# Kernel tuning notes

Hardware: AMD Instinct MI355X
Metric: run time of the kernel (lower is better)

Reference implementation:

```python
import jax, jax.numpy as jnp
import numpy as np

WIDTH = 1024
HEAD = 64


def setup_inputs() -> dict:
    key = jax.random.key(0)
    ks = jax.random.split(key, 8)
    B, S = 8, 2048
    x = jax.random.normal(ks[0], (B, S, WIDTH), dtype=jnp.float32)
    attn_mask = jnp.ones((B, S), dtype=jnp.int32)
    s = WIDTH ** -0.5
    Wq = jax.random.normal(ks[1], (WIDTH, HEAD), dtype=jnp.float32) * s
    bq = jnp.zeros((HEAD,), dtype=jnp.float32)
    Wk = jax.random.normal(ks[2], (WIDTH, HEAD), dtype=jnp.float32) * s
    bk = jnp.zeros((HEAD,), dtype=jnp.float32)
    Wv = jax.random.normal(ks[3], (WIDTH, HEAD), dtype=jnp.float32) * s
    bv = jnp.zeros((HEAD,), dtype=jnp.float32)
    return {"x": x, "attn_mask": attn_mask, "Wq": Wq, "bq": bq,
            "Wk": Wk, "bk": bk, "Wv": Wv, "bv": bv}


def reference(x, attn_mask, Wq, bq, Wk, bk, Wv, bv):
    # x: [B, S, width]; attn_mask: [B, S] (key padding mask)
    scale = HEAD ** -0.5
    Q = x @ Wq + bq  # [B, S, H]
    K = x @ Wk + bk
    V = x @ Wv + bv
    scores = jnp.einsum('bqh,bkh->bqk', Q, K) * scale  # [B, S, S]
    mask = (attn_mask[:, None, :] != 0)  # [B, 1, S] broadcast over queries
    scores = jnp.where(mask, scores, -jnp.inf)
    A = jax.nn.softmax(scores, axis=-1)
    return jnp.einsum('bqk,bkh->bqh', A, V)
```

## Files before the change

kernel.cpp:

```cpp
#include <hip/hip_runtime.h>
#include <hip/hip_bf16.h>

#define BATCH 8
#define SEQ   2048
#define DMODEL 1024
#define HD    64

typedef __attribute__((ext_vector_type(8))) short bf16x8;
typedef __attribute__((ext_vector_type(4))) float f32x4;
typedef __attribute__((ext_vector_type(4))) int int4v;
typedef __attribute__((ext_vector_type(2))) unsigned uint2v;
typedef unsigned int u32;

__device__ inline unsigned short f2bf(float f) {
    unsigned u = __builtin_bit_cast(unsigned, f);
    unsigned r = (u + 0x7FFFu + ((u >> 16) & 1u)) >> 16;
    return (unsigned short)r;
}

__device__ inline unsigned cvtpk(float lo, float hi) {
    unsigned r;
    asm("v_cvt_pk_bf16_f32 %0, %1, %2" : "=v"(r) : "v"(lo), "v"(hi));
    return r;
}

__device__ inline void gl_lds16(const void* g, void* l) {
    __builtin_amdgcn_global_load_lds(
        (const __attribute__((address_space(1))) u32*)g,
        (__attribute__((address_space(3))) u32*)l, 16, 0, 0);
}

__global__ void prep_w(const float* __restrict__ Wq, const float* __restrict__ Wk,
                       const float* __restrict__ Wv, unsigned short* __restrict__ WFrag) {
    __shared__ float tt[64][65];
    int p = blockIdx.x >> 4;
    int t = blockIdx.x & 15;
    int k0 = t * 64;
    const float* W = (p == 0) ? Wq : (p == 1) ? Wk : Wv;
    int tid = threadIdx.x;
#pragma unroll
    for (int j = 0; j < 16; j++) {
        int idx = tid + j * 256;
        int r = idx >> 6, c = idx & 63;
        tt[r][c] = W[(size_t)(k0 + r) * HD + c];
    }
    __syncthreads();
#pragma unroll
    for (int gi = 0; gi < 2; gi++) {
        int g = tid * 2 + gi;
        int ln = g & 15, lg = (g >> 4) & 3, s = (g >> 6) & 1, n = (g >> 7) & 3;
        union { bf16x8 v; unsigned short u[8]; } pk;
#pragma unroll
        for (int e = 0; e < 8; e++)
            pk.u[e] = f2bf(tt[s * 32 + lg * 8 + e][n * 16 + ln]);
        *(bf16x8*)(WFrag + (((size_t)(p * 4 + n) * 16 + t) * 1024 + s * 512 + lg * 128 + ln * 8)) = pk.v;
    }
}

__global__ __launch_bounds__(256, 2) void proj_kernel(
    const float* __restrict__ x,
    const float* __restrict__ bq, const float* __restrict__ bk, const float* __restrict__ bv,
    const unsigned short* __restrict__ WFrag,
    unsigned short* __restrict__ Q, unsigned short* __restrict__ K,
    unsigned short* __restrict__ VT) {

    __shared__ __align__(16) unsigned short Xls[32 * 1024];

    int tid = threadIdx.x;
    int w = tid >> 6, lane = tid & 63;
    int lg = lane >> 4, ln = lane & 15;
    int m0 = blockIdx.x * 32;

    const unsigned short* wbase[3];
#pragma unroll
    for (int j = 0; j < 3; j++)
        wbase[j] = WFrag + (size_t)(w * 3 + j) * 16384 + lane * 8;

#pragma unroll
    for (int j = 0; j < 16; j++) {
        int c = tid + j * 256;
        int row = c >> 7, slot = c & 127;
        const float* src = x + (size_t)(m0 + row) * DMODEL + slot * 8;
        f32x4 p0 = *(const f32x4*)(src);
        f32x4 p1 = *(const f32x4*)(src + 4);
        union { bf16x8 v; unsigned u[4]; } pk;
        pk.u[0] = cvtpk(p0[0], p0[1]); pk.u[1] = cvtpk(p0[2], p0[3]);
        pk.u[2] = cvtpk(p1[0], p1[1]); pk.u[3] = cvtpk(p1[2], p1[3]);
        *(bf16x8*)((char*)Xls + row * 2048 + ((slot ^ (row & 15)) << 4)) = pk.v;
    }

    f32x4 acc[2][3];
#pragma unroll
    for (int m = 0; m < 2; m++)
#pragma unroll
        for (int j = 0; j < 3; j++) acc[m][j] = (f32x4){0.f, 0.f, 0.f, 0.f};

    bf16x8 bA[6], bB[6];

    auto LB = [&](bf16x8* d, int t) {
#pragma unroll
        for (int s = 0; s < 2; s++)
#pragma unroll
            for (int j = 0; j < 3; j++)
                d[s * 3 + j] = *(const bf16x8*)(wbase[j] + t * 1024 + s * 512);
    };
    auto CP = [&](const bf16x8* bd, int t) {
        const char* xb = (const char*)Xls;
#pragma unroll
        for (int s = 0; s < 2; s++) {
            int slot0 = t * 8 + s * 4 + lg;
            bf16x8 a0 = *(const bf16x8*)(xb + ln * 2048 + ((slot0 ^ ln) << 4));
            bf16x8 a1 = *(const bf16x8*)(xb + (16 + ln) * 2048 + ((slot0 ^ ln) << 4));
#pragma unroll
            for (int j = 0; j < 3; j++) {
                acc[0][j] = __builtin_amdgcn_mfma_f32_16x16x32_bf16(a0, bd[s * 3 + j], acc[0][j], 0, 0, 0);
                acc[1][j] = __builtin_amdgcn_mfma_f32_16x16x32_bf16(a1, bd[s * 3 + j], acc[1][j], 0, 0, 0);
            }
        }
    };

    LB(bA, 0);
    __syncthreads();

#pragma unroll 1
    for (int t = 0; t < 16; t += 2) {
        LB(bB, t + 1);
        CP(bA, t);
        if (t + 2 < 16) LB(bA, t + 2);
        CP(bB, t + 1);
    }

#pragma unroll
    for (int j = 0; j < 3; j++) {
        int f = w * 3 + j;
        int p = f >> 2, n = f & 3;
        int col = n * 16 + ln;
        const float* bias = (p == 0) ? bq : (p == 1) ? bk : bv;
        float bb = bias[col];
#pragma unroll
        for (int m = 0; m < 2; m++) {
#pragma unroll
            for (int r = 0; r < 4; r++) {
                float v = acc[m][j][r] + bb;
                int grow = m0 + m * 16 + lg * 4 + r;
                if (p == 0)      Q[(size_t)grow * HD + col] = f2bf(v);
                else if (p == 1) K[(size_t)grow * HD + col] = f2bf(v);
                else {
                    int b2 = grow >> 11, srow = grow & (SEQ - 1);
                    VT[((size_t)b2 * HD + col) * SEQ + srow] = f2bf(v);
                }
            }
        }
    }
}

__device__ inline void stage_tile(int tid, const unsigned short* Kb, const unsigned short* VTb,
                                  int kt, unsigned short* kbuf, unsigned short* vbuf) {
#pragma unroll
    for (int i = 0; i < 2; i++) {
        int d = tid * 16 + i * 4096;
        int row = d >> 7, slot = (d >> 4) & 7;
        const unsigned short* src = Kb + (size_t)(kt + row) * HD + ((slot ^ (row & 7)) << 3);
        gl_lds16(src, (char*)kbuf + d);
    }
#pragma unroll
    for (int i = 0; i < 2; i++) {
        int d = tid * 16 + i * 4096;
        int row = d >> 7, slot = (d >> 4) & 7;
        const unsigned short* src = VTb + (size_t)row * SEQ + kt + ((slot ^ (row & 7)) << 3);
        gl_lds16(src, (char*)vbuf + d);
    }
}

__global__ __launch_bounds__(256, 4) void attn_kernel(
    const unsigned short* __restrict__ Q, const unsigned short* __restrict__ K,
    const unsigned short* __restrict__ VT, const int* __restrict__ mask,
    float* __restrict__ out,
    unsigned short* __restrict__ Op, float* __restrict__ Mp, float* __restrict__ Lp,
    int nsplit) {

    __shared__ __align__(16) unsigned short Kls[2][64 * 64];
    __shared__ __align__(16) unsigned short Vls[2][64 * 64];
    __shared__ __align__(16) unsigned short plds_[4][16 * 64];

    int tid = threadIdx.x;
    int w = tid >> 6, lane = tid & 63;
    int lg = lane >> 4, ln = lane & 15;
    int b = blockIdx.y;
    int kh = blockIdx.z;
    int q0 = blockIdx.x * 64 + w * 16;
    int ntiles = 32 / nsplit;
    int kt0 = kh * ntiles * 64;

    const float SC = 0.125f * 1.44269504088896f;

    const int* mb = mask + b * SEQ;

    bf16x8 qf[2];
    {
        const unsigned short* qptr = Q + ((size_t)b * SEQ + q0 + ln) * HD + lg * 8;
        qf[0] = *(const bf16x8*)(qptr);
        qf[1] = *(const bf16x8*)(qptr + 32);
    }

    f32x4 o[4];
#pragma unroll
    for (int n = 0; n < 4; n++) o[n] = (f32x4){0.f, 0.f, 0.f, 0.f};
    float mrun = -1e38f, lrun = 0.f;

    const unsigned short* Kb = K + (size_t)b * SEQ * HD;
    const unsigned short* VTb = VT + (size_t)b * HD * SEQ;

    unsigned short* kcur = &Kls[0][0]; unsigned short* knx = &Kls[1][0];
    unsigned short* vcur = &Vls[0][0]; unsigned short* vnx = &Vls[1][0];
    char* pl = (char*)&plds_[w][0];
    const int swz = (ln & 7) << 4;

    stage_tile(tid, Kb, VTb, kt0, kcur, vcur);
    __syncthreads();

#pragma unroll 2
    for (int tt = 0; tt < ntiles; ++tt) {
        int kt = kt0 + tt * 64;
        if (tt < ntiles - 1) stage_tile(tid, Kb, VTb, kt + 64, knx, vnx);

        int4v mi[4];
#pragma unroll
        for (int n = 0; n < 4; ++n)
            mi[n] = *(const int4v*)(mb + kt + n * 16 + lg * 4);

        f32x4 st[4];
        const char* kb = (const char*)kcur;
        __builtin_amdgcn_s_setprio(1);
#pragma unroll
        for (int n = 0; n < 4; ++n) {
            int rb = (n * 16 + ln) * 128;
            bf16x8 ka0 = *(const bf16x8*)(kb + ((rb + lg * 16) ^ swz));
            bf16x8 ka1 = *(const bf16x8*)(kb + ((rb + 64 + lg * 16) ^ swz));
            f32x4 z = (f32x4){0.f, 0.f, 0.f, 0.f};
            st[n] = __builtin_amdgcn_mfma_f32_16x16x32_bf16(ka0, qf[0], z, 0, 0, 0);
            st[n] = __builtin_amdgcn_mfma_f32_16x16x32_bf16(ka1, qf[1], st[n], 0, 0, 0);
        }
        __builtin_amdgcn_s_setprio(0);

#pragma unroll
        for (int n = 0; n < 4; ++n)
#pragma unroll
            for (int r = 0; r < 4; ++r)
                st[n][r] = fmaf(st[n][r], SC, mi[n][r] ? 0.f : -1e30f);

        f32x4 mx = st[0];
#pragma unroll
        for (int n = 1; n < 4; ++n)
#pragma unroll
            for (int r = 0; r < 4; ++r) mx[r] = fmaxf(mx[r], st[n][r]);
        float pmax = fmaxf(fmaxf(mx[0], mx[1]), fmaxf(mx[2], mx[3]));
        pmax = fmaxf(pmax, __shfl_xor(pmax, 16));
        pmax = fmaxf(pmax, __shfl_xor(pmax, 32));

        if (!__all(pmax <= mrun + 8.f)) {
            float mnew = fmaxf(mrun, pmax);
            float corr = exp2f(mrun - mnew);
            mrun = mnew;
            lrun *= corr;
            float c0 = __shfl(corr, lg * 4 + 0);
            float c1 = __shfl(corr, lg * 4 + 1);
            float c2 = __shfl(corr, lg * 4 + 2);
            float c3 = __shfl(corr, lg * 4 + 3);
#pragma unroll
            for (int n = 0; n < 4; ++n) {
                o[n][0] *= c0; o[n][1] *= c1; o[n][2] *= c2; o[n][3] *= c3;
            }
        }

        f32x4 sv = (f32x4){0.f, 0.f, 0.f, 0.f};
#pragma unroll
        for (int n = 0; n < 4; ++n)
#pragma unroll
            for (int r = 0; r < 4; ++r) {
                float pp = exp2f(st[n][r] - mrun);
                st[n][r] = pp;
                sv[r] += pp;
            }
        float ts = (sv[0] + sv[1]) + (sv[2] + sv[3]);
        ts += __shfl_xor(ts, 16);
        ts += __shfl_xor(ts, 32);
        lrun += ts;

#pragma unroll
        for (int n = 0; n < 4; ++n) {
            uint2v ww;
            ww[0] = cvtpk(st[n][0], st[n][1]);
            ww[1] = cvtpk(st[n][2], st[n][3]);
            *(uint2v*)(pl + ((ln * 128 + n * 32 + lg * 8) ^ swz)) = ww;
        }
        asm volatile("s_waitcnt lgkmcnt(0)" ::: "memory");
        __builtin_amdgcn_sched_barrier(0);
        bf16x8 pa0 = *(const bf16x8*)(pl + ((ln * 128 + lg * 16) ^ swz));
        bf16x8 pa1 = *(const bf16x8*)(pl + ((ln * 128 + 64 + lg * 16) ^ swz));

        const char* vb = (const char*)vcur;
        __builtin_amdgcn_s_setprio(1);
#pragma unroll
        for (int n = 0; n < 4; ++n) {
            int rb = (n * 16 + ln) * 128;
            bf16x8 v0 = *(const bf16x8*)(vb + ((rb + lg * 16) ^ swz));
            bf16x8 v1 = *(const bf16x8*)(vb + ((rb + 64 + lg * 16) ^ swz));
            o[n] = __builtin_amdgcn_mfma_f32_16x16x32_bf16(pa0, v0, o[n], 0, 0, 0);
            o[n] = __builtin_amdgcn_mfma_f32_16x16x32_bf16(pa1, v1, o[n], 0, 0, 0);
        }
        __builtin_amdgcn_s_setprio(0);

        __syncthreads();
        unsigned short* tk = kcur; kcur = knx; knx = tk;
        unsigned short* tv = vcur; vcur = vnx; vnx = tv;
    }

    if (nsplit == 1) {
#pragma unroll
        for (int r = 0; r < 4; r++) {
            float Lr = __shfl(lrun, lg * 4 + r);
            float inv = 1.0f / Lr;
            int row = q0 + lg * 4 + r;
#pragma unroll
            for (int n = 0; n < 4; n++)
                out[((size_t)b * SEQ + row) * HD + n * 16 + ln] = o[n][r] * inv;
        }
    } else {
        size_t base = (size_t)kh * BATCH * SEQ * HD;
#pragma unroll
        for (int r = 0; r < 4; r++) {
            int row = q0 + lg * 4 + r;
            size_t gr = (size_t)b * SEQ + row;
#pragma unroll
            for (int n = 0; n < 4; n++)
                Op[base + gr * HD + n * 16 + ln] = f2bf(o[n][r]);
        }
        if (lane < 16) {
            size_t gr = (size_t)b * SEQ + q0 + ln;
            Mp[(size_t)kh * BATCH * SEQ + gr] = mrun;
            Lp[(size_t)kh * BATCH * SEQ + gr] = lrun;
        }
    }
}

__global__ __launch_bounds__(256) void combine_kernel(
    const unsigned short* __restrict__ Op, const float* __restrict__ Mp,
    const float* __restrict__ Lp, float* __restrict__ out) {
    int g = blockIdx.x * 256 + threadIdx.x;
    int row = g >> 3;
    int c0 = (g & 7) * 8;
    const int NR = BATCH * SEQ;

    float m[4], l[4];
#pragma unroll
    for (int s = 0; s < 4; s++) {
        m[s] = Mp[(size_t)s * NR + row];
        l[s] = Lp[(size_t)s * NR + row];
    }
    float M = fmaxf(fmaxf(m[0], m[1]), fmaxf(m[2], m[3]));
    float e[4], L = 0.f;
#pragma unroll
    for (int s = 0; s < 4; s++) { e[s] = exp2f(m[s] - M); L += l[s] * e[s]; }
    float inv = 1.0f / L;

    float acc[8] = {0.f, 0.f, 0.f, 0.f, 0.f, 0.f, 0.f, 0.f};
#pragma unroll
    for (int s = 0; s < 4; s++) {
        bf16x8 ov = *(const bf16x8*)(Op + ((size_t)s * NR + row) * HD + c0);
#pragma unroll
        for (int i = 0; i < 8; i++) {
            float f = __builtin_bit_cast(float, ((u32)(unsigned short)ov[i]) << 16);
            acc[i] += f * e[s];
        }
    }
    f32x4 r0, r1;
#pragma unroll
    for (int i = 0; i < 4; i++) { r0[i] = acc[i] * inv; r1[i] = acc[4 + i] * inv; }
    *(f32x4*)(out + (size_t)row * HD + c0) = r0;
    *(f32x4*)(out + (size_t)row * HD + c0 + 4) = r1;
}

extern "C" void kernel_launch(void* const* d_in, const int* in_sizes, int n_in,
                              void* d_out, int out_size, void* d_ws, size_t ws_size,
                              hipStream_t stream) {
    const float* x  = (const float*)d_in[0];
    const int*   am = (const int*)d_in[1];
    const float* Wq = (const float*)d_in[2];
    const float* bq = (const float*)d_in[3];
    const float* Wk = (const float*)d_in[4];
    const float* bk = (const float*)d_in[5];
    const float* Wv = (const float*)d_in[6];
    const float* bv = (const float*)d_in[7];
    float* out = (float*)d_out;

    unsigned short* ws = (unsigned short*)d_ws;
    unsigned short* Wt  = ws;
    unsigned short* Qw  = ws + 3 * HD * DMODEL;
    unsigned short* Kw  = Qw + (size_t)BATCH * SEQ * HD;
    unsigned short* VTw = Kw + (size_t)BATCH * SEQ * HD;
    size_t base_sh = 3 * HD * DMODEL + 3 * (size_t)BATCH * SEQ * HD;
    unsigned short* Op = ws + base_sh;
    float* Mp = (float*)(Op + 4 * (size_t)BATCH * SEQ * HD);
    float* Lp = Mp + 4 * (size_t)BATCH * SEQ;
    size_t need = base_sh * 2 + 4 * (size_t)BATCH * SEQ * HD * 2
                + 8 * (size_t)BATCH * SEQ * 4;

    int nsplit = (ws_size >= need) ? 4 : 1;

    prep_w<<<48, 256, 0, stream>>>(Wq, Wk, Wv, Wt);
    proj_kernel<<<(BATCH * SEQ) / 32, 256, 0, stream>>>(x, bq, bk, bv, Wt, Qw, Kw, VTw);
    attn_kernel<<<dim3(SEQ / 64, BATCH, nsplit), 256, 0, stream>>>(Qw, Kw, VTw, am, out,
                                                                   Op, Mp, Lp, nsplit);
    if (nsplit == 4)
        combine_kernel<<<(BATCH * SEQ * 8) / 256, 256, 0, stream>>>(Op, Mp, Lp, out);
}
```

Measured before the change: 56.43 us.

## Split x conversion into separate kernel producing MFMA fragment layout for projection

Moves the fp32-to-bf16 conversion of x out of the projection kernel into a new conv_x kernel that writes x in pre-swizzled MFMA fragment order to workspace. The projection GEMM then loads A fragments directly from global memory with register double-buffering, dropping its 64KB LDS tile and block barrier, which may raise occupancy. The cost is an extra kernel launch plus a write and reread of a 32MB bf16 copy of x, and the larger workspace requirement may force nsplit=1 if the workspace is too small.

```diff
diff --git a/kernel.cpp b/kernel.cpp
--- a/kernel.cpp
+++ b/kernel.cpp
@@ -57,15 +57,42 @@
     }
 }
 
-__global__ __launch_bounds__(256, 2) void proj_kernel(
-    const float* __restrict__ x,
+__global__ __launch_bounds__(256) void conv_x(const float* __restrict__ x,
+                                              unsigned short* __restrict__ XFrag) {
+    __shared__ float t[16][260];
+    int mr16 = blockIdx.x >> 2;
+    int cc = blockIdx.x & 3;
+    int tid = threadIdx.x;
+#pragma unroll
+    for (int j = 0; j < 4; j++) {
+        int flat = tid + j * 256;
+        int row = flat >> 6;
+        int c4 = (flat & 63) << 2;
+        f32x4 v = *(const f32x4*)(x + (size_t)(mr16 * 16 + row) * DMODEL + cc * 256 + c4);
+        t[row][c4] = v[0]; t[row][c4 + 1] = v[1]; t[row][c4 + 2] = v[2]; t[row][c4 + 3] = v[3];
+    }
+    __syncthreads();
+#pragma unroll
+    for (int gi = 0; gi < 2; gi++) {
+        int g = tid + gi * 256;
+        int ln = g & 15, lg = (g >> 4) & 3, s = (g >> 6) & 1, tt = (g >> 7) & 3;
+        int kl = tt * 64 + s * 32 + lg * 8;
+        union { bf16x8 v; unsigned u[4]; } pk;
+#pragma unroll
+        for (int i = 0; i < 4; i++)
+            pk.u[i] = cvtpk(t[ln][kl + 2 * i], t[ln][kl + 2 * i + 1]);
+        *(bf16x8*)(XFrag + (((size_t)(mr16 * 16 + cc * 4 + tt) * 2 + s) * 512
+                            + (size_t)(lg * 16 + ln) * 8)) = pk.v;
+    }
+}
+
+__global__ __launch_bounds__(256, 2) void proj_gemm(
+    const unsigned short* __restrict__ XFrag,
     const float* __restrict__ bq, const float* __restrict__ bk, const float* __restrict__ bv,
     const unsigned short* __restrict__ WFrag,
     unsigned short* __restrict__ Q, unsigned short* __restrict__ K,
     unsigned short* __restrict__ VT) {
 
-    __shared__ __align__(16) unsigned short Xls[32 * 1024];
-
     int tid = threadIdx.x;
     int w = tid >> 6, lane = tid & 63;
     int lg = lane >> 4, ln = lane & 15;
@@ -75,19 +102,10 @@
 #pragma unroll
     for (int j = 0; j < 3; j++)
         wbase[j] = WFrag + (size_t)(w * 3 + j) * 16384 + lane * 8;
-
-#pragma unroll
-    for (int j = 0; j < 16; j++) {
-        int c = tid + j * 256;
-        int row = c >> 7, slot = c & 127;
-        const float* src = x + (size_t)(m0 + row) * DMODEL + slot * 8;
-        f32x4 p0 = *(const f32x4*)(src);
-        f32x4 p1 = *(const f32x4*)(src + 4);
-        union { bf16x8 v; unsigned u[4]; } pk;
-        pk.u[0] = cvtpk(p0[0], p0[1]); pk.u[1] = cvtpk(p0[2], p0[3]);
-        pk.u[2] = cvtpk(p1[0], p1[1]); pk.u[3] = cvtpk(p1[2], p1[3]);
-        *(bf16x8*)((char*)Xls + row * 2048 + ((slot ^ (row & 15)) << 4)) = pk.v;
-    }
+    const unsigned short* xf[2];
+#pragma unroll
+    for (int m = 0; m < 2; m++)
+        xf[m] = XFrag + (size_t)(blockIdx.x * 2 + m) * 16384 + lane * 8;
 
     f32x4 acc[2][3];
 #pragma unroll
@@ -95,7 +113,7 @@
 #pragma unroll
         for (int j = 0; j < 3; j++) acc[m][j] = (f32x4){0.f, 0.f, 0.f, 0.f};
 
-    bf16x8 bA[6], bB[6];
+    bf16x8 bA[6], bB[6], aA[4], aB[4];
 
     auto LB = [&](bf16x8* d, int t) {
 #pragma unroll
@@ -104,30 +122,35 @@
             for (int j = 0; j < 3; j++)
                 d[s * 3 + j] = *(const bf16x8*)(wbase[j] + t * 1024 + s * 512);
     };
-    auto CP = [&](const bf16x8* bd, int t) {
-        const char* xb = (const char*)Xls;
-#pragma unroll
-        for (int s = 0; s < 2; s++) {
-            int slot0 = t * 8 + s * 4 + lg;
-            bf16x8 a0 = *(const bf16x8*)(xb + ln * 2048 + ((slot0 ^ ln) << 4));
-            bf16x8 a1 = *(const bf16x8*)(xb + (16 + ln) * 2048 + ((slot0 ^ ln) << 4));
+    auto LA = [&](bf16x8* d, int t) {
+#pragma unroll
+        for (int s = 0; s < 2; s++)
+#pragma unroll
+            for (int m = 0; m < 2; m++)
+                d[s * 2 + m] = *(const bf16x8*)(xf[m] + (t * 2 + s) * 512);
+    };
+    auto CP = [&](const bf16x8* ad, const bf16x8* bd) {
+#pragma unroll
+        for (int s = 0; s < 2; s++)
 #pragma unroll
             for (int j = 0; j < 3; j++) {
-                acc[0][j] = __builtin_amdgcn_mfma_f32_16x16x32_bf16(a0, bd[s * 3 + j], acc[0][j], 0, 0, 0);
-                acc[1][j] = __builtin_amdgcn_mfma_f32_16x16x32_bf16(a1, bd[s * 3 + j], acc[1][j], 0, 0, 0);
+                acc[0][j] = __builtin_amdgcn_mfma_f32_16x16x32_bf16(ad[s * 2 + 0], bd[s * 3 + j], acc[0][j], 0, 0, 0);
+                acc[1][j] = __builtin_amdgcn_mfma_f32_16x16x32_bf16(ad[s * 2 + 1], bd[s * 3 + j], acc[1][j], 0, 0, 0);
             }
-        }
     };
 
+    LA(aA, 0);
     LB(bA, 0);
-    __syncthreads();
-
 #pragma unroll 1
     for (int t = 0; t < 16; t += 2) {
+        LA(aB, t + 1);
         LB(bB, t + 1);
-        CP(bA, t);
-        if (t + 2 < 16) LB(bA, t + 2);
-        CP(bB, t + 1);
+        CP(aA, bA);
+        if (t + 2 < 16) {
+            LA(aA, t + 2);
+            LB(bA, t + 2);
+        }
+        CP(aB, bB);
     }
 
 #pragma unroll
@@ -403,13 +426,16 @@
     unsigned short* Op = ws + base_sh;
     float* Mp = (float*)(Op + 4 * (size_t)BATCH * SEQ * HD);
     float* Lp = Mp + 4 * (size_t)BATCH * SEQ;
+    unsigned short* XFrag = (unsigned short*)(Lp + 4 * (size_t)BATCH * SEQ);
     size_t need = base_sh * 2 + 4 * (size_t)BATCH * SEQ * HD * 2
-                + 8 * (size_t)BATCH * SEQ * 4;
+                + 8 * (size_t)BATCH * SEQ * 4
+                + (size_t)BATCH * SEQ * DMODEL * 2;
 
     int nsplit = (ws_size >= need) ? 4 : 1;
 
     prep_w<<<48, 256, 0, stream>>>(Wq, Wk, Wv, Wt);
-    proj_kernel<<<(BATCH * SEQ) / 32, 256, 0, stream>>>(x, bq, bk, bv, Wt, Qw, Kw, VTw);
+    conv_x<<<(BATCH * SEQ / 16) * 4, 256, 0, stream>>>(x, XFrag);
+    proj_gemm<<<(BATCH * SEQ) / 32, 256, 0, stream>>>(XFrag, bq, bk, bv, Wt, Qw, Kw, VTw);
     attn_kernel<<<dim3(SEQ / 64, BATCH, nsplit), 256, 0, stream>>>(Qw, Kw, VTw, am, out,
                                                                    Op, Mp, Lp, nsplit);
     if (nsplit == 4)
```

Measured after the change: 69.08 us. +22.4%, slower.

## Stage fp32 x tiles directly to LDS and convert to bf16 at MFMA operand load

Applied to the files above, without the earlier changes.

The projection kernel no longer loads x into registers, converts to bf16 and writes LDS. It uses a direct global-to-LDS copy (gl_lds16) of fp32 data in two K-halves with an XOR swizzle, and converts to bf16 when reading MFMA A operands. This is meant to cut register pressure and VGPR round-trips during staging. In exchange it doubles the LDS reads per operand, repeats the conversion for each wave, and adds a barrier between the halves with no overlap between staging and compute.

```diff
diff --git a/kernel.cpp b/kernel.cpp
--- a/kernel.cpp
+++ b/kernel.cpp
@@ -64,7 +64,7 @@
     unsigned short* __restrict__ Q, unsigned short* __restrict__ K,
     unsigned short* __restrict__ VT) {
 
-    __shared__ __align__(16) unsigned short Xls[32 * 1024];
+    __shared__ __align__(16) float Xf[32 * 512];
 
     int tid = threadIdx.x;
     int w = tid >> 6, lane = tid & 63;
@@ -76,19 +76,6 @@
     for (int j = 0; j < 3; j++)
         wbase[j] = WFrag + (size_t)(w * 3 + j) * 16384 + lane * 8;
 
-#pragma unroll
-    for (int j = 0; j < 16; j++) {
-        int c = tid + j * 256;
-        int row = c >> 7, slot = c & 127;
-        const float* src = x + (size_t)(m0 + row) * DMODEL + slot * 8;
-        f32x4 p0 = *(const f32x4*)(src);
-        f32x4 p1 = *(const f32x4*)(src + 4);
-        union { bf16x8 v; unsigned u[4]; } pk;
-        pk.u[0] = cvtpk(p0[0], p0[1]); pk.u[1] = cvtpk(p0[2], p0[3]);
-        pk.u[2] = cvtpk(p1[0], p1[1]); pk.u[3] = cvtpk(p1[2], p1[3]);
-        *(bf16x8*)((char*)Xls + row * 2048 + ((slot ^ (row & 15)) << 4)) = pk.v;
-    }
-
     f32x4 acc[2][3];
 #pragma unroll
     for (int m = 0; m < 2; m++)
@@ -97,37 +84,57 @@
 
     bf16x8 bA[6], bB[6];
 
-    auto LB = [&](bf16x8* d, int t) {
+    auto STAGE = [&](int kh) {
+#pragma unroll
+        for (int i = 0; i < 16; i++) {
+            int d = tid * 16 + i * 4096;
+            int row = d >> 11, p = (d >> 4) & 127;
+            gl_lds16(x + (size_t)(m0 + row) * DMODEL + kh * 512 + ((p ^ (row & 15)) << 2),
+                     (char*)Xf + d);
+        }
+    };
+    auto LB = [&](bf16x8* d, int tg) {
 #pragma unroll
         for (int s = 0; s < 2; s++)
 #pragma unroll
             for (int j = 0; j < 3; j++)
-                d[s * 3 + j] = *(const bf16x8*)(wbase[j] + t * 1024 + s * 512);
+                d[s * 3 + j] = *(const bf16x8*)(wbase[j] + tg * 1024 + s * 512);
     };
     auto CP = [&](const bf16x8* bd, int t) {
-        const char* xb = (const char*)Xls;
+        const char* xb = (const char*)Xf;
 #pragma unroll
         for (int s = 0; s < 2; s++) {
-            int slot0 = t * 8 + s * 4 + lg;
-            bf16x8 a0 = *(const bf16x8*)(xb + ln * 2048 + ((slot0 ^ ln) << 4));
-            bf16x8 a1 = *(const bf16x8*)(xb + (16 + ln) * 2048 + ((slot0 ^ ln) << 4));
+            int q = t * 16 + s * 8 + lg * 2;
+            f32x4 v0 = *(const f32x4*)(xb + ln * 2048 + ((q ^ ln) << 4));
+            f32x4 v1 = *(const f32x4*)(xb + ln * 2048 + (((q + 1) ^ ln) << 4));
+            f32x4 v2 = *(const f32x4*)(xb + (16 + ln) * 2048 + ((q ^ ln) << 4));
+            f32x4 v3 = *(const f32x4*)(xb + (16 + ln) * 2048 + (((q + 1) ^ ln) << 4));
+            union { bf16x8 v; unsigned u[4]; } a0, a1;
+            a0.u[0] = cvtpk(v0[0], v0[1]); a0.u[1] = cvtpk(v0[2], v0[3]);
+            a0.u[2] = cvtpk(v1[0], v1[1]); a0.u[3] = cvtpk(v1[2], v1[3]);
+            a1.u[0] = cvtpk(v2[0], v2[1]); a1.u[1] = cvtpk(v2[2], v2[3]);
+            a1.u[2] = cvtpk(v3[0], v3[1]); a1.u[3] = cvtpk(v3[2], v3[3]);
 #pragma unroll
             for (int j = 0; j < 3; j++) {
-                acc[0][j] = __builtin_amdgcn_mfma_f32_16x16x32_bf16(a0, bd[s * 3 + j], acc[0][j], 0, 0, 0);
-                acc[1][j] = __builtin_amdgcn_mfma_f32_16x16x32_bf16(a1, bd[s * 3 + j], acc[1][j], 0, 0, 0);
+                acc[0][j] = __builtin_amdgcn_mfma_f32_16x16x32_bf16(a0.v, bd[s * 3 + j], acc[0][j], 0, 0, 0);
+                acc[1][j] = __builtin_amdgcn_mfma_f32_16x16x32_bf16(a1.v, bd[s * 3 + j], acc[1][j], 0, 0, 0);
             }
         }
     };
 
-    LB(bA, 0);
-    __syncthreads();
-
 #pragma unroll 1
-    for (int t = 0; t < 16; t += 2) {
-        LB(bB, t + 1);
-        CP(bA, t);
-        if (t + 2 < 16) LB(bA, t + 2);
-        CP(bB, t + 1);
+    for (int kh = 0; kh < 2; kh++) {
+        STAGE(kh);
+        LB(bA, kh * 8);
+        __syncthreads();
+#pragma unroll 1
+        for (int t = 0; t < 8; t += 2) {
+            LB(bB, kh * 8 + t + 1);
+            CP(bA, t);
+            if (t + 2 < 8) LB(bA, kh * 8 + t + 2);
+            CP(bB, t + 1);
+        }
+        __syncthreads();
     }
 
 #pragma unroll
```

Result: slower. 61.39 us (+8.8%).
